# Optimization experiments

Measured on AMD Instinct MI355X. Metric: run time of the kernel, lower is better.

Reference implementation:

```python
import jax, jax.numpy as jnp
import numpy as np

B, C_IN, C_OUT, K, H, W = 8, 512, 512, 3, 32, 32
EPS = 1e-8


def _fir_filter():
    f1 = jnp.array([1.0, 3.0, 3.0, 1.0], dtype=jnp.float32)
    f = jnp.outer(f1, f1)
    f = f / f.sum()
    return f * 4.0  # gain = 2**2, filter.ndim/2 == 1


def setup_inputs() -> dict:
    key = jax.random.key(0)
    k1, k2, k3 = jax.random.split(key, 3)
    x = jax.random.normal(k1, (B, C_IN, H, W), dtype=jnp.float32)
    styles = jax.random.normal(k2, (B, C_IN), dtype=jnp.float32)
    w = jax.random.normal(k3, (C_OUT, C_IN, K, K), dtype=jnp.float32)  # lr_multiplier=1
    return {"x": x, "styles": styles, "w": w}


def reference(x, styles, w):
    batch = x.shape[0]
    gain = 1.0 / np.sqrt(C_OUT * C_IN * K * K)
    # modulate: [B, O, I, kh, kw]
    wm = (w[None] * gain) * (styles[:, None, :, None, None] + 1.0)
    # demodulate
    dcoefs = jax.lax.rsqrt(jnp.sum(wm * wm, axis=(2, 3, 4)) + EPS)  # [B, O]
    wm = wm * dcoefs[:, :, None, None, None]
    # fused modconv: batch folded into channels/groups
    x1 = x.reshape(1, batch * C_IN, H, W)
    # torch conv_transpose2d(stride=2, padding=0, groups=B) == dilated conv with
    # spatially flipped kernel, lhs_dilation=2, padding=K-1 on each side.
    w_eq = jnp.flip(wm, axis=(-2, -1)).reshape(batch * C_OUT, C_IN, K, K)
    y = jax.lax.conv_general_dilated(
        x1, w_eq,
        window_strides=(1, 1),
        padding=[(K - 1, K - 1), (K - 1, K - 1)],
        lhs_dilation=(2, 2),
        feature_group_count=batch,
        dimension_numbers=("NCHW", "OIHW", "NCHW"),
    )  # [1, B*O, 2H+1, 2W+1]
    # Upfirdn2d: up=1, down=1, pad=[1,1,1,1], depthwise 4x4 FIR (cross-correlation;
    # filter is symmetric so no flip needed)
    C = batch * C_OUT
    f = jnp.broadcast_to(_fir_filter()[None, None], (C, 1, 4, 4))
    y = jax.lax.conv_general_dilated(
        y, f,
        window_strides=(1, 1),
        padding=[(1, 1), (1, 1)],
        feature_group_count=C,
        dimension_numbers=("NCHW", "OIHW", "NCHW"),
    )  # [1, B*O, 2H, 2W]
    return y.reshape(batch, C_OUT, 2 * H, 2 * W)
```

## Files before the change

### kernel.cpp

```cpp
#include <hip/hip_runtime.h>
#include <stdint.h>


#define DI __device__ __forceinline__

typedef __bf16 bf16x8 __attribute__((ext_vector_type(8)));
typedef float f32x4 __attribute__((ext_vector_type(4)));

DI float bf2f(ushort u) { union { uint32_t i; float f; } v; v.i = ((uint32_t)u) << 16; return v.f; }
DI ushort f2bf(float f) {
  union { float f; uint32_t i; } v; v.f = f;
  uint32_t x = v.i;
  return (ushort)((x + 0x7FFFu + ((x >> 16) & 1u)) >> 16);
}

#define GAIN (1.0f / 1536.0f)

__global__ __launch_bounds__(256) void k_prep(const float* __restrict__ w,
                                              const float* __restrict__ styles,
                                              const float* __restrict__ x,
                                              ushort* __restrict__ Wm,
                                              ushort* __restrict__ xt) {
  __shared__ union {
    struct { float ss[4096]; float dc[8]; float wred[4][8]; } wp;
    float tl[32][257];
  } sm;
  const int t = threadIdx.x;
  if (blockIdx.x < 512) {
    const int o = blockIdx.x;
#pragma unroll
    for (int j = 0; j < 4; j++) {
      const int idx = (t + j * 256) * 4;
      *(float4*)&sm.wp.ss[idx] = *(const float4*)&styles[idx];
    }
    float wreg[18];
    const float* wp_ = w + o * 4608 + t * 18;
#pragma unroll
    for (int k = 0; k < 9; k++) {
      float2 v2 = *(const float2*)(wp_ + 2 * k);
      wreg[2 * k] = v2.x;
      wreg[2 * k + 1] = v2.y;
    }
    float q0 = 0.f, q1 = 0.f;
#pragma unroll
    for (int k = 0; k < 9; k++) {
      q0 += wreg[k] * wreg[k];
      q1 += wreg[9 + k] * wreg[9 + k];
    }
    __syncthreads();
    float pb[8];
#pragma unroll
    for (int b = 0; b < 8; b++) {
      float s0 = sm.wp.ss[b * 512 + 2 * t] + 1.0f;
      float s1 = sm.wp.ss[b * 512 + 2 * t + 1] + 1.0f;
      pb[b] = s0 * s0 * q0 + s1 * s1 * q1;
    }
#pragma unroll
    for (int b = 0; b < 8; b++)
#pragma unroll
      for (int off = 32; off > 0; off >>= 1) pb[b] += __shfl_down(pb[b], off, 64);
    const int wid = t >> 6, lane = t & 63;
    if (lane == 0) {
#pragma unroll
      for (int b = 0; b < 8; b++) sm.wp.wred[wid][b] = pb[b];
    }
    __syncthreads();
    if (t < 8)
      sm.wp.dc[t] = rsqrtf((sm.wp.wred[0][t] + sm.wp.wred[1][t] + sm.wp.wred[2][t] + sm.wp.wred[3][t]) *
                               (GAIN * GAIN) + 1e-8f);
    __syncthreads();
#pragma unroll
    for (int b = 0; b < 8; b++) {
      const float d = sm.wp.dc[b];
      const float s0 = GAIN * (sm.wp.ss[b * 512 + 2 * t] + 1.0f) * d;
      const float s1 = GAIN * (sm.wp.ss[b * 512 + 2 * t + 1] + 1.0f) * d;
      ushort* base = Wm + ((size_t)(b * 9) * 512 + o) * 512 + 2 * t;
#pragma unroll
      for (int tap = 0; tap < 9; tap++) {
        ushort2 val = make_ushort2(f2bf(wreg[tap] * s0), f2bf(wreg[9 + tap] * s1));
        *(ushort2*)(base + (size_t)tap * 262144) = val;
      }
    }
  } else {
    const int idx = blockIdx.x - 512;
    const int hw0 = (idx & 3) * 256, i0 = ((idx >> 2) & 15) * 32, b = idx >> 6;
    const float* xb = x + b * (512 * 1024);
#pragma unroll
    for (int p = 0; p < 8; p++) {
      const int r = p * 4 + (t >> 6);
      const int c4 = (t & 63) * 4;
      float4 v = *(const float4*)&xb[(i0 + r) * 1024 + hw0 + c4];
      sm.tl[r][c4] = v.x; sm.tl[r][c4 + 1] = v.y; sm.tl[r][c4 + 2] = v.z; sm.tl[r][c4 + 3] = v.w;
    }
    __syncthreads();
    ushort* xtb = xt + b * (1024 * 512);
#pragma unroll
    for (int p = 0; p < 8; p++) {
      const int hw = p * 32 + (t >> 3);
      const int i4 = (t & 7) * 4;
      ushort4 v = make_ushort4(f2bf(sm.tl[i4][hw]), f2bf(sm.tl[i4 + 1][hw]),
                               f2bf(sm.tl[i4 + 2][hw]), f2bf(sm.tl[i4 + 3][hw]));
      *(ushort4*)&xtb[(hw0 + hw) * 512 + i0 + i4] = v;
    }
  }
}

__global__ __launch_bounds__(256) void k_gemm(const ushort* __restrict__ A,
                                              const ushort* __restrict__ Bt,
                                              ushort* __restrict__ C) {
  __shared__ __attribute__((aligned(16))) char smem[34816];
  const int id = blockIdx.x;
  const int batch = id & 7;
  const int rem = id >> 3;
  const int tap = rem >> 5;
  const int t = rem & 31;
  const int mt = t >> 3, nt = t & 7;
  const int g = batch * 9 + tap;
  const ushort* Ag = A + g * (512 * 512);
  const ushort* Bg = Bt + batch * (1024 * 512);
  ushort* Cg = C + g * (512 * 1024);
  const int tid = threadIdx.x;
  const int lane = tid & 63, wv = tid >> 6;
  const int m0 = mt * 128, n0 = nt * 128;
  const int wm2 = wv >> 1, wn2 = wv & 1;
  const int lq = lane >> 4, l15 = lane & 15;
  const int l4 = lane & 3, ld4 = lane >> 2;
  const int r0 = (0 * 4 + wv) * 16 + ld4;
  const int r1 = (1 * 4 + wv) * 16 + ld4;

  const ushort* pA0 = Ag + (m0 + r0) * 512 + l4 * 8;
  const ushort* pA1 = Ag + (m0 + r1) * 512 + l4 * 8;
  const ushort* pB0 = Bg + (n0 + r0) * 512 + l4 * 8;
  const ushort* pB1 = Bg + (n0 + r1) * 512 + l4 * 8;
  char* dA0 = smem + (0 * 4 + wv) * 1024;
  char* dA1 = smem + (1 * 4 + wv) * 1024;
  char* dB0 = smem + 8192 + (0 * 4 + wv) * 1024;
  char* dB1 = smem + 8192 + (1 * 4 + wv) * 1024;

#define ISSUE(buf, kc)                                                                        \
  do {                                                                                        \
    __builtin_amdgcn_global_load_lds((const __attribute__((address_space(1))) void*)(pA0 + (kc)), \
                                     (__attribute__((address_space(3))) void*)(dA0 + (buf)*16384), 16, 0, 0); \
    __builtin_amdgcn_global_load_lds((const __attribute__((address_space(1))) void*)(pA1 + (kc)), \
                                     (__attribute__((address_space(3))) void*)(dA1 + (buf)*16384), 16, 0, 0); \
    __builtin_amdgcn_global_load_lds((const __attribute__((address_space(1))) void*)(pB0 + (kc)), \
                                     (__attribute__((address_space(3))) void*)(dB0 + (buf)*16384), 16, 0, 0); \
    __builtin_amdgcn_global_load_lds((const __attribute__((address_space(1))) void*)(pB1 + (kc)), \
                                     (__attribute__((address_space(3))) void*)(dB1 + (buf)*16384), 16, 0, 0); \
  } while (0)

  const char* abase = smem + (wm2 * 64 + l15) * 64 + lq * 16;
  const char* bbase = smem + 8192 + (wn2 * 64 + l15) * 64 + lq * 16;

  f32x4 zero = {0.f, 0.f, 0.f, 0.f};
  f32x4 acc[4][4];
#pragma unroll
  for (int mi = 0; mi < 4; mi++)
#pragma unroll
    for (int ni = 0; ni < 4; ni++) acc[mi][ni] = zero;

  ISSUE(0, 0);
  for (int it = 0; it < 16; ++it) {
    __syncthreads();
    const int cur = it & 1;
    if (it < 15) ISSUE(cur ^ 1, (it + 1) * 32);
    const int bo = cur * 16384;
    bf16x8 af[4], bfr[4];
#pragma unroll
    for (int mi = 0; mi < 4; mi++) af[mi] = *(const bf16x8*)(abase + bo + mi * 1024);
#pragma unroll
    for (int ni = 0; ni < 4; ni++) bfr[ni] = *(const bf16x8*)(bbase + bo + ni * 1024);
#pragma unroll
    for (int mi = 0; mi < 4; mi++)
#pragma unroll
      for (int ni = 0; ni < 4; ni++)
        acc[mi][ni] = __builtin_amdgcn_mfma_f32_16x16x32_bf16(af[mi], bfr[ni], acc[mi][ni], 0, 0, 0);
  }
#undef ISSUE
  __syncthreads();
  ushort* cs = (ushort*)smem;
#pragma unroll
  for (int mi = 0; mi < 4; mi++) {
#pragma unroll
    for (int ni = 0; ni < 4; ni++) {
      const int row = wm2 * 64 + mi * 16 + lq * 4;
      const int col = wn2 * 64 + ni * 16 + l15;
      f32x4 v = acc[mi][ni];
#pragma unroll
      for (int r = 0; r < 4; r++) cs[(row + r) * 136 + col] = f2bf(v[r]);
    }
  }
  __syncthreads();
#pragma unroll
  for (int p = 0; p < 8; p++) {
    const int r2 = p * 16 + (tid >> 4);
    const int c8 = (tid & 15) * 8;
    *(uint4*)(Cg + (m0 + r2) * 1024 + n0 + c8) = *(const uint4*)(cs + r2 * 136 + c8);
  }
}

__global__ __launch_bounds__(512) void k_fir(const ushort* __restrict__ C,
                                             float* __restrict__ out) {
  const int bo = blockIdx.x;
  const int b = bo >> 9, o = bo & 511;
  __shared__ __attribute__((aligned(16))) ushort Ct[9 * 1024];
  __shared__ float V[3 * 64 * 36];
  const ushort* Cb = C + ((size_t)(b * 9) * 512 + o) * 1024;
  for (int c = threadIdx.x; c < 1152; c += 512) {
    const int tap = c >> 7, off = (c & 127) * 8;
    *(uint4*)&Ct[tap * 1024 + off] = *(const uint4*)&Cb[(size_t)tap * 524288 + off];
  }
  __syncthreads();
#pragma unroll
  for (int j = 0; j < 3; j++) {
    const int gidx = threadIdx.x + j * 512;
    const int kw = gidx >> 9;
    const int rem = gidx & 511;
    const int u = rem >> 3;
    const int w0 = (rem & 7) * 4;
    float a0 = 0.f, a1 = 0.f, a2 = 0.f, a3 = 0.f;
#pragma unroll
    for (int kh = 0; kh < 3; kh++) {
      const int s0 = (kh + 1 + u) & 1;
#pragma unroll
      for (int d = 0; d < 2; d++) {
        const int h = (u + s0 + 2 * d - 1 - kh) >> 1;
        const bool ok = (h >= 0) & (h < 32);
        const float cf = ok ? ((s0 == d) ? 1.f : 3.f) : 0.f;
        const int hh = ok ? h : 0;
        const uint2 cv = *(const uint2*)&Ct[kh * 3072 + kw * 1024 + hh * 32 + w0];
        a0 += cf * bf2f((ushort)(cv.x & 0xffff));
        a1 += cf * bf2f((ushort)(cv.x >> 16));
        a2 += cf * bf2f((ushort)(cv.y & 0xffff));
        a3 += cf * bf2f((ushort)(cv.y >> 16));
      }
    }
    *(float4*)&V[kw * 2304 + u * 36 + w0] = make_float4(a0, a1, a2, a3);
  }
  __syncthreads();
  const size_t ob = (size_t)bo * 4096;
#pragma unroll
  for (int j = 0; j < 2; j++) {
    const int px4 = threadIdx.x + j * 512;
    const int u = px4 >> 4;
    const int v0 = (px4 & 15) * 4;
    float r[4] = {0.f, 0.f, 0.f, 0.f};
#pragma unroll
    for (int q = 0; q < 4; q++) {
      const int v = v0 + q;
#pragma unroll
      for (int kw = 0; kw < 3; kw++) {
        const int t0 = (kw + 1 + v) & 1;
#pragma unroll
        for (int d = 0; d < 2; d++) {
          const int wx = (v + t0 + 2 * d - 1 - kw) >> 1;
          const bool ok = (wx >= 0) & (wx < 32);
          const float cf = ok ? ((t0 == d) ? 1.f : 3.f) : 0.f;
          const int ww = ok ? wx : 0;
          r[q] += cf * V[kw * 2304 + u * 36 + ww];
        }
      }
      r[q] *= 0.0625f;
    }
    *(float4*)&out[ob + u * 64 + v0] = make_float4(r[0], r[1], r[2], r[3]);
  }
}

extern "C" void kernel_launch(void* const* d_in, const int* in_sizes, int n_in,
                              void* d_out, int out_size, void* d_ws, size_t ws_size,
                              hipStream_t stream) {
  (void)in_sizes; (void)n_in; (void)out_size; (void)ws_size;
  const float* x = (const float*)d_in[0];
  const float* styles = (const float*)d_in[1];
  const float* w = (const float*)d_in[2];
  float* out = (float*)d_out;
  char* ws = (char*)d_ws;
  ushort* Wm = (ushort*)ws;
  ushort* XT = (ushort*)(ws + 37748736);
  ushort* C = (ushort*)(ws + 37748736 + 8388608);

  k_prep<<<1024, 256, 0, stream>>>(w, styles, x, Wm, XT);
  k_gemm<<<2304, 256, 0, stream>>>(Wm, XT, C);
  k_fir<<<4096, 512, 0, stream>>>(C, out);
}
```

Before: 162.2 us.

## Rewrite GEMM with 256x256 tiles, 8 waves, swizzled LDS and phased pipeline

Replaces the 128x128, 4-wave GEMM with a 256x256 tile, 8-wave kernel that uses 64-wide K steps, XOR-swizzled LDS layout, double-buffered global_load_lds staging interleaved across four MFMA phases, explicit vmcnt waits and s_setprio around MFMA bursts. The larger tile raises arithmetic intensity and cuts redundant global loads, and the swizzle avoids LDS bank conflicts. In exchange it uses 128KB LDS and many accumulators per block, leaving only 576 blocks, which may limit occupancy and fill the GPU's CUs poorly.

New measurement: 165.6 us. +2.1%, slower.

```diff
diff --git a/kernel.cpp b/kernel.cpp
--- a/kernel.cpp
+++ b/kernel.cpp
@@ -105,98 +105,181 @@
   }
 }
 
-__global__ __launch_bounds__(256) void k_gemm(const ushort* __restrict__ A,
-                                              const ushort* __restrict__ Bt,
-                                              ushort* __restrict__ C) {
-  __shared__ __attribute__((aligned(16))) char smem[34816];
+__global__ __launch_bounds__(512, 2) void k_gemm(const ushort* __restrict__ A,
+                                                 const ushort* __restrict__ Bt,
+                                                 ushort* __restrict__ C) {
+  __shared__ __attribute__((aligned(128))) char smem[131072];
   const int id = blockIdx.x;
   const int batch = id & 7;
   const int rem = id >> 3;
-  const int tap = rem >> 5;
-  const int t = rem & 31;
-  const int mt = t >> 3, nt = t & 7;
-  const int g = batch * 9 + tap;
-  const ushort* Ag = A + g * (512 * 512);
-  const ushort* Bg = Bt + batch * (1024 * 512);
-  ushort* Cg = C + g * (512 * 1024);
+  const int tap = rem >> 3;
+  const int t8 = rem & 7;
+  const int mt = t8 >> 2, nt = t8 & 3;
+  const int m0 = mt * 256, n0 = nt * 256;
+  const ushort* Ag = A + (size_t)(batch * 9 + tap) * (512 * 512);
+  const ushort* Bg = Bt + (size_t)batch * (1024 * 512);
+  ushort* Cg = C + (size_t)(batch * 9 + tap) * (512 * 1024);
+
   const int tid = threadIdx.x;
-  const int lane = tid & 63, wv = tid >> 6;
-  const int m0 = mt * 128, n0 = nt * 128;
-  const int wm2 = wv >> 1, wn2 = wv & 1;
-  const int lq = lane >> 4, l15 = lane & 15;
-  const int l4 = lane & 3, ld4 = lane >> 2;
-  const int r0 = (0 * 4 + wv) * 16 + ld4;
-  const int r1 = (1 * 4 + wv) * 16 + ld4;
-
-  const ushort* pA0 = Ag + (m0 + r0) * 512 + l4 * 8;
-  const ushort* pA1 = Ag + (m0 + r1) * 512 + l4 * 8;
-  const ushort* pB0 = Bg + (n0 + r0) * 512 + l4 * 8;
-  const ushort* pB1 = Bg + (n0 + r1) * 512 + l4 * 8;
-  char* dA0 = smem + (0 * 4 + wv) * 1024;
-  char* dA1 = smem + (1 * 4 + wv) * 1024;
-  char* dB0 = smem + 8192 + (0 * 4 + wv) * 1024;
-  char* dB1 = smem + 8192 + (1 * 4 + wv) * 1024;
-
-#define ISSUE(buf, kc)                                                                        \
-  do {                                                                                        \
-    __builtin_amdgcn_global_load_lds((const __attribute__((address_space(1))) void*)(pA0 + (kc)), \
-                                     (__attribute__((address_space(3))) void*)(dA0 + (buf)*16384), 16, 0, 0); \
-    __builtin_amdgcn_global_load_lds((const __attribute__((address_space(1))) void*)(pA1 + (kc)), \
-                                     (__attribute__((address_space(3))) void*)(dA1 + (buf)*16384), 16, 0, 0); \
-    __builtin_amdgcn_global_load_lds((const __attribute__((address_space(1))) void*)(pB0 + (kc)), \
-                                     (__attribute__((address_space(3))) void*)(dB0 + (buf)*16384), 16, 0, 0); \
-    __builtin_amdgcn_global_load_lds((const __attribute__((address_space(1))) void*)(pB1 + (kc)), \
-                                     (__attribute__((address_space(3))) void*)(dB1 + (buf)*16384), 16, 0, 0); \
+  const int w = tid >> 6, lane = tid & 63;
+  const int wm = w >> 2, wn = w & 3;
+  const int lq = lane >> 4, l15 = lane & 15, l7 = lane & 7;
+  const int rlow = lane >> 3;
+  const int ssw = (lane & 7) ^ rlow;
+
+  const char* pA = (const char*)Ag + (size_t)(m0 + w * 8 + rlow) * 1024 + ssw * 16;
+  const char* pB = (const char*)Bg + (size_t)(n0 + w * 8 + rlow) * 1024 + ssw * 16;
+  char* sAd = smem + w * 1024;
+  char* sBd = smem + 32768 + w * 1024;
+
+#define GLL(srcp, dstp)                                                                     \
+  __builtin_amdgcn_global_load_lds((const __attribute__((address_space(1))) void*)(srcp),   \
+                                   (__attribute__((address_space(3))) void*)(dstp), 16, 0, 0)
+#define STAGE_A(buf, h, kt)                                                                 \
+  do {                                                                                      \
+    GLL(pA + (h) * 131072 + (kt) * 128,         sAd + (buf) * 65536 + (h) * 16384);         \
+    GLL(pA + (h) * 131072 + 65536 + (kt) * 128, sAd + (buf) * 65536 + (h) * 16384 + 8192);  \
   } while (0)
-
-  const char* abase = smem + (wm2 * 64 + l15) * 64 + lq * 16;
-  const char* bbase = smem + 8192 + (wn2 * 64 + l15) * 64 + lq * 16;
-
-  f32x4 zero = {0.f, 0.f, 0.f, 0.f};
-  f32x4 acc[4][4];
-#pragma unroll
-  for (int mi = 0; mi < 4; mi++)
-#pragma unroll
-    for (int ni = 0; ni < 4; ni++) acc[mi][ni] = zero;
-
-  ISSUE(0, 0);
-  for (int it = 0; it < 16; ++it) {
-    __syncthreads();
-    const int cur = it & 1;
-    if (it < 15) ISSUE(cur ^ 1, (it + 1) * 32);
-    const int bo = cur * 16384;
-    bf16x8 af[4], bfr[4];
-#pragma unroll
-    for (int mi = 0; mi < 4; mi++) af[mi] = *(const bf16x8*)(abase + bo + mi * 1024);
-#pragma unroll
-    for (int ni = 0; ni < 4; ni++) bfr[ni] = *(const bf16x8*)(bbase + bo + ni * 1024);
-#pragma unroll
-    for (int mi = 0; mi < 4; mi++)
-#pragma unroll
-      for (int ni = 0; ni < 4; ni++)
-        acc[mi][ni] = __builtin_amdgcn_mfma_f32_16x16x32_bf16(af[mi], bfr[ni], acc[mi][ni], 0, 0, 0);
-  }
-#undef ISSUE
-  __syncthreads();
+#define STAGE_B(buf, h, kt)                                                                 \
+  do {                                                                                      \
+    GLL(pB + (h) * 131072 + (kt) * 128,         sBd + (buf) * 65536 + (h) * 16384);         \
+    GLL(pB + (h) * 131072 + 65536 + (kt) * 128, sBd + (buf) * 65536 + (h) * 16384 + 8192);  \
+  } while (0)
+#define CF asm volatile("" ::: "memory")
+#define BAR()                          \
+  do {                                 \
+    CF;                                \
+    __builtin_amdgcn_s_barrier();      \
+    CF;                                \
+  } while (0)
+
+  const char* Ard = smem + wm * 16384 + l15 * 128;
+  const char* Brd = smem + 32768 + (wn >> 1) * 16384 + (wn & 1) * 8192 + l15 * 128;
+  const int s0o = (lq ^ l7) * 16;
+  const int s1o = ((4 + lq) ^ l7) * 16;
+
+  f32x4 acc[8][4];
+  const f32x4 z4 = {0.f, 0.f, 0.f, 0.f};
+#pragma unroll
+  for (int i = 0; i < 8; ++i)
+#pragma unroll
+    for (int n = 0; n < 4; ++n) acc[i][n] = z4;
+
+  STAGE_A(0, 0, 0); STAGE_A(0, 1, 0); STAGE_B(0, 0, 0); STAGE_B(0, 1, 0);
+  STAGE_A(1, 0, 1); STAGE_A(1, 1, 1); STAGE_B(1, 0, 1); STAGE_B(1, 1, 1);
+  asm volatile("s_waitcnt vmcnt(8)" ::: "memory");
+  BAR();
+
+#pragma unroll
+  for (int t = 0; t < 8; ++t) {
+    const int buf = t & 1;
+    const char* Ab = Ard + buf * 65536;
+    const char* Bb = Brd + buf * 65536;
+    bf16x8 a[4][2], b[4][2];
+#pragma unroll
+    for (int i = 0; i < 4; ++i) {
+      a[i][0] = *(const bf16x8*)(Ab + i * 2048 + s0o);
+      a[i][1] = *(const bf16x8*)(Ab + i * 2048 + s1o);
+    }
+#pragma unroll
+    for (int n = 0; n < 2; ++n) {
+      b[n][0] = *(const bf16x8*)(Bb + n * 2048 + s0o);
+      b[n][1] = *(const bf16x8*)(Bb + n * 2048 + s1o);
+    }
+    BAR();
+    __builtin_amdgcn_s_setprio(1);
+#pragma unroll
+    for (int n = 0; n < 2; ++n)
+#pragma unroll
+      for (int i = 0; i < 4; ++i) {
+        acc[i][n] = __builtin_amdgcn_mfma_f32_16x16x32_bf16(a[i][0], b[n][0], acc[i][n], 0, 0, 0);
+        acc[i][n] = __builtin_amdgcn_mfma_f32_16x16x32_bf16(a[i][1], b[n][1], acc[i][n], 0, 0, 0);
+      }
+    __builtin_amdgcn_s_setprio(0);
+    BAR();
+#pragma unroll
+    for (int n = 2; n < 4; ++n) {
+      b[n][0] = *(const bf16x8*)(Bb + n * 2048 + s0o);
+      b[n][1] = *(const bf16x8*)(Bb + n * 2048 + s1o);
+    }
+    BAR();
+    __builtin_amdgcn_s_setprio(1);
+#pragma unroll
+    for (int n = 2; n < 4; ++n)
+#pragma unroll
+      for (int i = 0; i < 4; ++i) {
+        acc[i][n] = __builtin_amdgcn_mfma_f32_16x16x32_bf16(a[i][0], b[n][0], acc[i][n], 0, 0, 0);
+        acc[i][n] = __builtin_amdgcn_mfma_f32_16x16x32_bf16(a[i][1], b[n][1], acc[i][n], 0, 0, 0);
+      }
+    __builtin_amdgcn_s_setprio(0);
+    BAR();
+    bf16x8 a2[4][2];
+#pragma unroll
+    for (int i = 0; i < 4; ++i) {
+      a2[i][0] = *(const bf16x8*)(Ab + (4 + i) * 2048 + s0o);
+      a2[i][1] = *(const bf16x8*)(Ab + (4 + i) * 2048 + s1o);
+    }
+    if (t < 6) { STAGE_B(buf, 0, t + 2); STAGE_B(buf, 1, t + 2); }
+    BAR();
+    __builtin_amdgcn_s_setprio(1);
+#pragma unroll
+    for (int n = 0; n < 2; ++n)
+#pragma unroll
+      for (int i = 0; i < 4; ++i) {
+        acc[4 + i][n] = __builtin_amdgcn_mfma_f32_16x16x32_bf16(a2[i][0], b[n][0], acc[4 + i][n], 0, 0, 0);
+        acc[4 + i][n] = __builtin_amdgcn_mfma_f32_16x16x32_bf16(a2[i][1], b[n][1], acc[4 + i][n], 0, 0, 0);
+      }
+    __builtin_amdgcn_s_setprio(0);
+    BAR();
+    if (t < 6) { STAGE_A(buf, 0, t + 2); STAGE_A(buf, 1, t + 2); }
+    BAR();
+    __builtin_amdgcn_s_setprio(1);
+#pragma unroll
+    for (int n = 2; n < 4; ++n)
+#pragma unroll
+      for (int i = 0; i < 4; ++i) {
+        acc[4 + i][n] = __builtin_amdgcn_mfma_f32_16x16x32_bf16(a2[i][0], b[n][0], acc[4 + i][n], 0, 0, 0);
+        acc[4 + i][n] = __builtin_amdgcn_mfma_f32_16x16x32_bf16(a2[i][1], b[n][1], acc[4 + i][n], 0, 0, 0);
+      }
+    __builtin_amdgcn_s_setprio(0);
+    if (t < 6) {
+      asm volatile("s_waitcnt vmcnt(8)" ::: "memory");
+    } else if (t == 6) {
+      asm volatile("s_waitcnt vmcnt(0)" ::: "memory");
+    }
+    BAR();
+  }
+
   ushort* cs = (ushort*)smem;
 #pragma unroll
-  for (int mi = 0; mi < 4; mi++) {
-#pragma unroll
-    for (int ni = 0; ni < 4; ni++) {
-      const int row = wm2 * 64 + mi * 16 + lq * 4;
-      const int col = wn2 * 64 + ni * 16 + l15;
-      f32x4 v = acc[mi][ni];
-#pragma unroll
-      for (int r = 0; r < 4; r++) cs[(row + r) * 136 + col] = f2bf(v[r]);
-    }
-  }
-  __syncthreads();
-#pragma unroll
-  for (int p = 0; p < 8; p++) {
-    const int r2 = p * 16 + (tid >> 4);
-    const int c8 = (tid & 15) * 8;
-    *(uint4*)(Cg + (m0 + r2) * 1024 + n0 + c8) = *(const uint4*)(cs + r2 * 136 + c8);
-  }
+  for (int p = 0; p < 2; ++p) {
+    if (p) BAR();
+    if (wm == p) {
+#pragma unroll
+      for (int mi2 = 0; mi2 < 8; ++mi2)
+#pragma unroll
+        for (int n = 0; n < 4; ++n) {
+          const int row = mi2 * 16 + lq * 4;
+          const int col = wn * 64 + n * 16 + l15;
+          const f32x4 v = acc[mi2][n];
+#pragma unroll
+          for (int r = 0; r < 4; ++r) cs[(row + r) * 264 + col] = f2bf(v[r]);
+        }
+    }
+    BAR();
+#pragma unroll
+    for (int j = 0; j < 8; ++j) {
+      const int idx = j * 512 + tid;
+      const int row = idx >> 5, c = idx & 31;
+      *(uint4*)(Cg + (size_t)(m0 + p * 128 + row) * 1024 + n0 + c * 8) =
+          *(const uint4*)(cs + row * 264 + c * 8);
+    }
+  }
+#undef GLL
+#undef STAGE_A
+#undef STAGE_B
+#undef CF
+#undef BAR
 }
 
 __global__ __launch_bounds__(512) void k_fir(const ushort* __restrict__ C,
@@ -280,6 +363,6 @@
   ushort* C = (ushort*)(ws + 37748736 + 8388608);
 
   k_prep<<<1024, 256, 0, stream>>>(w, styles, x, Wm, XT);
-  k_gemm<<<2304, 256, 0, stream>>>(Wm, XT, C);
+  k_gemm<<<576, 512, 0, stream>>>(Wm, XT, C);
   k_fir<<<4096, 512, 0, stream>>>(C, out);
 }
```
